# Performance work log

Hardware: AMD Instinct MI355X
Metric: run time of the kernel (lower is better)

Reference implementation:

```python
import jax, jax.numpy as jnp
import numpy as np

INPUT_DIM = 1024
OUTPUT_DIM = 1024
DEGREE = 8


def pentanacci_basis(x, degree):
    # x: [B, I] (already sigmoided). Returns [B, I, degree+1].
    # P0 = 0, P1 = 1, P2 = x, P3 = x, P4 = x^2,
    # Pn = x*P(n-1) + P(n-2) + P(n-3) + P(n-4) + P(n-5) for n >= 5
    zeros = jnp.zeros_like(x)
    ones = jnp.ones_like(x)
    seeds = [zeros, ones, x, x, x * x]
    basis = seeds[: degree + 1]
    for n in range(5, degree + 1):
        basis.append(x * basis[n - 1] + basis[n - 2] + basis[n - 3]
                     + basis[n - 4] + basis[n - 5])
    return jnp.stack(basis, axis=-1)


def setup_inputs() -> dict:
    key = jax.random.key(0)
    kx, kw = jax.random.split(key)
    x = jax.random.normal(kx, (4096, INPUT_DIM), dtype=jnp.float32)
    std = 1.0 / (INPUT_DIM * (DEGREE + 1))
    coeffs = std * jax.random.normal(kw, (INPUT_DIM, OUTPUT_DIM, DEGREE + 1),
                                     dtype=jnp.float32)
    return {"x": x, "coeffs": coeffs}


def reference(x, coeffs):
    degree = coeffs.shape[-1] - 1
    xs = jax.nn.sigmoid(x)                      # [B, I]
    basis = pentanacci_basis(xs, degree)        # [B, I, D+1]
    y = jnp.einsum('bid,iod->bo', basis, coeffs)  # [B, O]
    return y
```

## Files before the change

### kernel.cpp

```cpp
#include <hip/hip_runtime.h>
#include <stdint.h>

#define M_DIM 4096
#define I_DIM 1024
#define O_DIM 1024
#define KB 6
#define K_DIM (I_DIM * KB)
#define SPLITS 4

typedef __attribute__((ext_vector_type(8))) short short8;
typedef __attribute__((ext_vector_type(4))) float f32x4;
typedef __attribute__((ext_vector_type(4))) unsigned int u32x4;
typedef __attribute__((ext_vector_type(4))) float hfloat4;

__device__ __forceinline__ unsigned short f2bf(float f) {
  union { float f; unsigned int u; } v; v.f = f;
  unsigned int u = v.u;
  unsigned int r = (u + 0x7FFFu + ((u >> 16) & 1u)) >> 16;
  return (unsigned short)r;
}

__global__ __launch_bounds__(256) void k_basis(const float* __restrict__ x,
                                               unsigned short* __restrict__ A) {
  int t = blockIdx.x * 256 + threadIdx.x;
  long e0 = (long)t * 8;
  const hfloat4* xp = (const hfloat4*)(x + e0);
  hfloat4 v0 = xp[0], v1 = xp[1];
  float xv[8];
  xv[0]=v0[0]; xv[1]=v0[1]; xv[2]=v0[2]; xv[3]=v0[3];
  xv[4]=v1[0]; xv[5]=v1[1]; xv[6]=v1[2]; xv[7]=v1[3];
  unsigned short outv[48];
#pragma unroll
  for (int e = 0; e < 8; ++e) {
    float s  = 1.0f / (1.0f + __expf(-xv[e]));
    float b2 = s, b3 = s, b4 = s * s;
    float b5 = fmaf(s, b4, b3 + b2 + 1.0f);
    float b6 = fmaf(s, b5, b4 + b3 + b2 + 1.0f);
    float b7 = fmaf(s, b6, b5 + b4 + b3 + b2);
    float b8 = fmaf(s, b7, b6 + b5 + b4 + b3);
    outv[e*6+0] = f2bf(s);
    outv[e*6+1] = f2bf(b4);
    outv[e*6+2] = f2bf(b5);
    outv[e*6+3] = f2bf(b6);
    outv[e*6+4] = f2bf(b7);
    outv[e*6+5] = f2bf(b8);
  }
  u32x4* dst = (u32x4*)(A + e0 * KB);
  const u32x4* srcv = (const u32x4*)outv;
#pragma unroll
  for (int q = 0; q < 6; ++q) dst[q] = srcv[q];
}

__global__ __launch_bounds__(256) void k_coef(const float* __restrict__ C,
                                              unsigned short* __restrict__ Bt,
                                              float* __restrict__ partB) {
  __shared__ unsigned short tile[32 * 192];
  __shared__ float bred[256];
  int i0 = blockIdx.x * 32, o0 = blockIdx.y * 32;
  int t = threadIdx.x;
  int ol = t & 31, ig = t >> 5;
  float bsum = 0.f;
#pragma unroll
  for (int r = 0; r < 4; ++r) {
    int il = ig + r * 8;
    const float* p = C + (size_t)(i0 + il) * (O_DIM * 9) + (size_t)(o0 + ol) * 9;
    float c1 = p[1];
    float c2 = p[2], c3 = p[3], c4 = p[4], c5 = p[5], c6 = p[6], c7 = p[7], c8 = p[8];
    bsum += c1;
    unsigned short* q = &tile[ol * 192 + il * 6];
    q[0] = f2bf(c2 + c3);
    q[1] = f2bf(c4);
    q[2] = f2bf(c5);
    q[3] = f2bf(c6);
    q[4] = f2bf(c7);
    q[5] = f2bf(c8);
  }
  bred[t] = bsum;
  __syncthreads();
  if (t < 32) {
    float s = 0.f;
#pragma unroll
    for (int g = 0; g < 8; ++g) s += bred[g * 32 + t];
    partB[(size_t)blockIdx.x * O_DIM + o0 + t] = s;
  }
  const u32x4* lsrc = (const u32x4*)tile;
#pragma unroll
  for (int r = 0; r < 3; ++r) {
    int c = t + r * 256;
    int row = c / 24, off = c % 24;
    u32x4* gdst = (u32x4*)(Bt + (size_t)(o0 + row) * K_DIM + (size_t)i0 * 6 + off * 8);
    *gdst = lsrc[c];
  }
}

__global__ __launch_bounds__(256) void k_bias2(const float* __restrict__ partB,
                                               float* __restrict__ bias) {
  int o = blockIdx.x * 256 + threadIdx.x;
  float s = 0.f;
#pragma unroll
  for (int ib = 0; ib < 32; ++ib) s += partB[(size_t)ib * O_DIM + o];
  bias[o] = s;
}

#define SBAR __builtin_amdgcn_sched_barrier(0)

template<bool SPLIT>
__global__ __launch_bounds__(512, 2) void k_gemm8(const unsigned short* __restrict__ A,
                                                  const unsigned short* __restrict__ B,
                                                  const float* __restrict__ bias,
                                                  float* __restrict__ dst) {
  constexpr int CK = SPLIT ? (K_DIM / SPLITS) : K_DIM;
  constexpr int NT = CK / 64;
  constexpr int PPX = SPLIT ? 8 : 2;
  __shared__ char lds[131072];
  const int tid = threadIdx.x;
  const int lane = tid & 63, wid = tid >> 6;
  const int wm = wid >> 2, wn = wid & 3;
  const int l15 = lane & 15, lk = lane >> 4, l7 = lane & 7;
  const int flat = blockIdx.x + (blockIdx.y << 2) + (blockIdx.z << 6);
  const int xcd = flat & 7, slot = flat >> 3;
  const int panel = xcd * PPX + (slot >> 2);
  const int xn = slot & 3;
  const int ym = panel & 15, zk = panel >> 4;
  const int m0 = ym * 256, n0 = xn * 256;
  const size_t kb = (size_t)zk * CK;
  const int srow = tid >> 3;
  const int cg8 = (((tid & 7) ^ ((tid >> 3) & 7)) * 8);
  const int cx0 = (lk ^ l7) * 16;
  const int cx1 = ((4 + lk) ^ l7) * 16;
  const int arow = wm * 128 + l15;
  const int brow = wn * 64 + l15;

  auto gload = [&](const unsigned short* s, int ldsoff) {
    __builtin_amdgcn_global_load_lds((const __attribute__((address_space(1))) void*)s,
        (__attribute__((address_space(3))) void*)(lds + ldsoff), 16, 0, 0);
  };
  auto stageA = [&](int buf, int h, int kt2) {
    const unsigned short* s = A + (size_t)(m0 + h * 128 + srow) * K_DIM + kb + (size_t)kt2 * 64 + cg8;
    int d = buf * 65536 + h * 16384 + tid * 16;
    gload(s, d);
    gload(s + (size_t)64 * K_DIM, d + 8192);
  };
  auto stageB = [&](int buf, int h, int kt2) {
    const unsigned short* s = B + (size_t)(n0 + h * 128 + srow) * K_DIM + kb + (size_t)kt2 * 64 + cg8;
    int d = buf * 65536 + 32768 + h * 16384 + tid * 16;
    gload(s, d);
    gload(s + (size_t)64 * K_DIM, d + 8192);
  };

  short8 af[4][2], bf0[2][2], bf1[2][2];
  f32x4 acc[8][4];
#pragma unroll
  for (int i = 0; i < 8; ++i)
#pragma unroll
    for (int n = 0; n < 4; ++n)
#pragma unroll
      for (int j = 0; j < 4; ++j) acc[i][n][j] = 0.f;

  auto loadA = [&](int buf, int h) {
#pragma unroll
    for (int mm = 0; mm < 4; ++mm) {
      int rb = buf * 65536 + (arow + h * 64 + mm * 16) * 128;
      af[mm][0] = *(const short8*)(lds + rb + cx0);
      af[mm][1] = *(const short8*)(lds + rb + cx1);
    }
  };
  auto loadB = [&](int buf, int g, short8 (&bfx)[2][2]) {
#pragma unroll
    for (int nn = 0; nn < 2; ++nn) {
      int rb = buf * 65536 + 32768 + (brow + g * 32 + nn * 16) * 128;
      bfx[nn][0] = *(const short8*)(lds + rb + cx0);
      bfx[nn][1] = *(const short8*)(lds + rb + cx1);
    }
  };
  auto quad = [&](int h, int g, short8 (&bfx)[2][2]) {
#pragma unroll
    for (int mm = 0; mm < 4; ++mm)
#pragma unroll
      for (int nn = 0; nn < 2; ++nn)
#pragma unroll
        for (int kc = 0; kc < 2; ++kc)
          acc[h * 4 + mm][g * 2 + nn] =
              __builtin_amdgcn_mfma_f32_16x16x32_bf16(af[mm][kc], bfx[nn][kc],
                                                      acc[h * 4 + mm][g * 2 + nn], 0, 0, 0);
  };
  auto sync1 = [&]() {
    SBAR; __builtin_amdgcn_s_barrier();
    asm volatile("s_waitcnt lgkmcnt(0)" ::: "memory"); SBAR;
    __builtin_amdgcn_s_setprio(1);
  };
  auto endp = [&]() {
    __builtin_amdgcn_s_setprio(0); SBAR;
  };

  stageA(0, 0, 0); stageA(0, 1, 0); stageB(0, 0, 0); stageB(0, 1, 0);
  stageB(1, 0, 1); stageB(1, 1, 1);
  asm volatile("s_waitcnt vmcnt(4)" ::: "memory"); SBAR;
  __builtin_amdgcn_s_barrier(); SBAR;

#pragma unroll 1
  for (int kt = 0; kt < NT; ++kt) {
    const int buf = kt & 1, nb = buf ^ 1;
    loadA(buf, 0); loadB(buf, 0, bf0);
    if (kt + 1 < NT) stageA(nb, 1, kt + 1);
    sync1(); quad(0, 0, bf0); endp();
    loadB(buf, 1, bf1);
    if (kt + 1 < NT) stageA(nb, 0, kt + 1);
    sync1(); quad(0, 1, bf1); endp();
    loadA(buf, 1);
    if (kt + 2 < NT) stageB(buf, 0, kt + 2);
    sync1(); quad(1, 1, bf1); endp();
    if (kt + 2 < NT) stageB(buf, 1, kt + 2);
    sync1(); quad(1, 0, bf0); endp();
    if (kt + 1 < NT) {
      if (kt + 2 < NT) asm volatile("s_waitcnt vmcnt(4)" ::: "memory");
      else             asm volatile("s_waitcnt vmcnt(0)" ::: "memory");
      SBAR;
      __builtin_amdgcn_s_barrier(); SBAR;
    }
  }

  float* base = SPLIT ? (dst + (size_t)zk * ((size_t)M_DIM * O_DIM)) : dst;
#pragma unroll
  for (int mi = 0; mi < 8; ++mi) {
    int r0 = m0 + wm * 128 + mi * 16 + (lk << 2);
#pragma unroll
    for (int ni = 0; ni < 4; ++ni) {
      int col = n0 + wn * 64 + ni * 16 + l15;
      float bv = SPLIT ? 0.f : bias[col];
#pragma unroll
      for (int j = 0; j < 4; ++j)
        base[(size_t)(r0 + j) * O_DIM + col] = acc[mi][ni][j] + bv;
    }
  }
}

__global__ __launch_bounds__(256) void k_reduce(const float* __restrict__ part,
                                                const float* __restrict__ bias,
                                                float* __restrict__ out) {
  size_t t = (size_t)blockIdx.x * 256 + threadIdx.x;
  size_t idx = t * 4;
  const size_t P = (size_t)M_DIM * O_DIM;
  f32x4 s0 = *(const f32x4*)(part + idx);
  f32x4 s1 = *(const f32x4*)(part + P + idx);
  f32x4 s2 = *(const f32x4*)(part + 2 * P + idx);
  f32x4 s3 = *(const f32x4*)(part + 3 * P + idx);
  f32x4 bv = *(const f32x4*)(bias + (idx & (O_DIM - 1)));
  f32x4 r;
#pragma unroll
  for (int j = 0; j < 4; ++j) r[j] = ((s0[j] + s1[j]) + (s2[j] + s3[j])) + bv[j];
  *(f32x4*)(out + idx) = r;
}

extern "C" void kernel_launch(void* const* d_in, const int* in_sizes, int n_in,
                              void* d_out, int out_size, void* d_ws, size_t ws_size,
                              hipStream_t stream) {
  const float* x      = (const float*)d_in[0];
  const float* coeffs = (const float*)d_in[1];
  float* out = (float*)d_out;
  char* ws = (char*)d_ws;
  const size_t offA     = 0;
  const size_t offB     = 50331648;
  const size_t offBias  = offB + 12582912;
  const size_t offPartB = offBias + 4096;
  const size_t offPart  = offPartB + 131072;
  const size_t needSplit = offPart + (size_t)SPLITS * M_DIM * O_DIM * 4;

  unsigned short* A  = (unsigned short*)(ws + offA);
  unsigned short* Bt = (unsigned short*)(ws + offB);
  float* bias        = (float*)(ws + offBias);
  float* partB       = (float*)(ws + offPartB);
  float* part        = (float*)(ws + offPart);

  k_basis<<<2048, 256, 0, stream>>>(x, A);
  k_coef<<<dim3(32, 32), 256, 0, stream>>>(coeffs, Bt, partB);
  k_bias2<<<4, 256, 0, stream>>>(partB, bias);

  if (ws_size >= needSplit) {
    k_gemm8<true><<<dim3(O_DIM / 256, M_DIM / 256, SPLITS), 512, 0, stream>>>(A, Bt, bias, part);
    k_reduce<<<(M_DIM * O_DIM) / (256 * 4), 256, 0, stream>>>(part, bias, out);
  } else {
    k_gemm8<false><<<dim3(O_DIM / 256, M_DIM / 256, 1), 512, 0, stream>>>(A, Bt, bias, out);
  }
}
```

Baseline: 95.61 us.

## Store split-K partials in fp16 and merge basis/coef prep kernels

The split-K GEMM partial sums are now written as fp16 instead of fp32, halving the partial-buffer write and reduce-read traffic. The reduce kernel now handles 8 elements per thread with fp16 loads. Separately, the basis and coefficient preparation kernels are merged into one launch that branches on block index, removing a launch gap. Storing partials in fp16 loses precision and range in the intermediate sums.

```diff
diff --git a/kernel.cpp b/kernel.cpp
--- a/kernel.cpp
+++ b/kernel.cpp
@@ -12,6 +12,7 @@
 typedef __attribute__((ext_vector_type(4))) float f32x4;
 typedef __attribute__((ext_vector_type(4))) unsigned int u32x4;
 typedef __attribute__((ext_vector_type(4))) float hfloat4;
+typedef __attribute__((ext_vector_type(8))) _Float16 h16x8;
 
 __device__ __forceinline__ unsigned short f2bf(float f) {
   union { float f; unsigned int u; } v; v.f = f;
@@ -20,76 +21,79 @@
   return (unsigned short)r;
 }
 
-__global__ __launch_bounds__(256) void k_basis(const float* __restrict__ x,
-                                               unsigned short* __restrict__ A) {
-  int t = blockIdx.x * 256 + threadIdx.x;
-  long e0 = (long)t * 8;
-  const hfloat4* xp = (const hfloat4*)(x + e0);
-  hfloat4 v0 = xp[0], v1 = xp[1];
-  float xv[8];
-  xv[0]=v0[0]; xv[1]=v0[1]; xv[2]=v0[2]; xv[3]=v0[3];
-  xv[4]=v1[0]; xv[5]=v1[1]; xv[6]=v1[2]; xv[7]=v1[3];
-  unsigned short outv[48];
-#pragma unroll
-  for (int e = 0; e < 8; ++e) {
-    float s  = 1.0f / (1.0f + __expf(-xv[e]));
-    float b2 = s, b3 = s, b4 = s * s;
-    float b5 = fmaf(s, b4, b3 + b2 + 1.0f);
-    float b6 = fmaf(s, b5, b4 + b3 + b2 + 1.0f);
-    float b7 = fmaf(s, b6, b5 + b4 + b3 + b2);
-    float b8 = fmaf(s, b7, b6 + b5 + b4 + b3);
-    outv[e*6+0] = f2bf(s);
-    outv[e*6+1] = f2bf(b4);
-    outv[e*6+2] = f2bf(b5);
-    outv[e*6+3] = f2bf(b6);
-    outv[e*6+4] = f2bf(b7);
-    outv[e*6+5] = f2bf(b8);
-  }
-  u32x4* dst = (u32x4*)(A + e0 * KB);
-  const u32x4* srcv = (const u32x4*)outv;
-#pragma unroll
-  for (int q = 0; q < 6; ++q) dst[q] = srcv[q];
-}
-
-__global__ __launch_bounds__(256) void k_coef(const float* __restrict__ C,
+__global__ __launch_bounds__(256) void k_prep(const float* __restrict__ x,
+                                              const float* __restrict__ C,
+                                              unsigned short* __restrict__ A,
                                               unsigned short* __restrict__ Bt,
                                               float* __restrict__ partB) {
-  __shared__ unsigned short tile[32 * 192];
-  __shared__ float bred[256];
-  int i0 = blockIdx.x * 32, o0 = blockIdx.y * 32;
-  int t = threadIdx.x;
-  int ol = t & 31, ig = t >> 5;
-  float bsum = 0.f;
-#pragma unroll
-  for (int r = 0; r < 4; ++r) {
-    int il = ig + r * 8;
-    const float* p = C + (size_t)(i0 + il) * (O_DIM * 9) + (size_t)(o0 + ol) * 9;
-    float c1 = p[1];
-    float c2 = p[2], c3 = p[3], c4 = p[4], c5 = p[5], c6 = p[6], c7 = p[7], c8 = p[8];
-    bsum += c1;
-    unsigned short* q = &tile[ol * 192 + il * 6];
-    q[0] = f2bf(c2 + c3);
-    q[1] = f2bf(c4);
-    q[2] = f2bf(c5);
-    q[3] = f2bf(c6);
-    q[4] = f2bf(c7);
-    q[5] = f2bf(c8);
-  }
-  bred[t] = bsum;
-  __syncthreads();
-  if (t < 32) {
-    float s = 0.f;
-#pragma unroll
-    for (int g = 0; g < 8; ++g) s += bred[g * 32 + t];
-    partB[(size_t)blockIdx.x * O_DIM + o0 + t] = s;
-  }
-  const u32x4* lsrc = (const u32x4*)tile;
-#pragma unroll
-  for (int r = 0; r < 3; ++r) {
-    int c = t + r * 256;
-    int row = c / 24, off = c % 24;
-    u32x4* gdst = (u32x4*)(Bt + (size_t)(o0 + row) * K_DIM + (size_t)i0 * 6 + off * 8);
-    *gdst = lsrc[c];
+  const int bid = blockIdx.x;
+  if (bid < 2048) {
+    int t = bid * 256 + threadIdx.x;
+    long e0 = (long)t * 8;
+    const hfloat4* xp = (const hfloat4*)(x + e0);
+    hfloat4 v0 = xp[0], v1 = xp[1];
+    float xv[8];
+    xv[0]=v0[0]; xv[1]=v0[1]; xv[2]=v0[2]; xv[3]=v0[3];
+    xv[4]=v1[0]; xv[5]=v1[1]; xv[6]=v1[2]; xv[7]=v1[3];
+    unsigned short outv[48];
+#pragma unroll
+    for (int e = 0; e < 8; ++e) {
+      float s  = 1.0f / (1.0f + __expf(-xv[e]));
+      float b2 = s, b3 = s, b4 = s * s;
+      float b5 = fmaf(s, b4, b3 + b2 + 1.0f);
+      float b6 = fmaf(s, b5, b4 + b3 + b2 + 1.0f);
+      float b7 = fmaf(s, b6, b5 + b4 + b3 + b2);
+      float b8 = fmaf(s, b7, b6 + b5 + b4 + b3);
+      outv[e*6+0] = f2bf(s);
+      outv[e*6+1] = f2bf(b4);
+      outv[e*6+2] = f2bf(b5);
+      outv[e*6+3] = f2bf(b6);
+      outv[e*6+4] = f2bf(b7);
+      outv[e*6+5] = f2bf(b8);
+    }
+    u32x4* dst = (u32x4*)(A + e0 * KB);
+    const u32x4* srcv = (const u32x4*)outv;
+#pragma unroll
+    for (int q = 0; q < 6; ++q) dst[q] = srcv[q];
+  } else {
+    __shared__ unsigned short tile[32 * 192];
+    __shared__ float bred[256];
+    int b = bid - 2048;
+    int i0 = (b & 31) * 32, o0 = (b >> 5) * 32;
+    int t = threadIdx.x;
+    int ol = t & 31, ig = t >> 5;
+    float bsum = 0.f;
+#pragma unroll
+    for (int r = 0; r < 4; ++r) {
+      int il = ig + r * 8;
+      const float* p = C + (size_t)(i0 + il) * (O_DIM * 9) + (size_t)(o0 + ol) * 9;
+      float c1 = p[1];
+      float c2 = p[2], c3 = p[3], c4 = p[4], c5 = p[5], c6 = p[6], c7 = p[7], c8 = p[8];
+      bsum += c1;
+      unsigned short* q = &tile[ol * 192 + il * 6];
+      q[0] = f2bf(c2 + c3);
+      q[1] = f2bf(c4);
+      q[2] = f2bf(c5);
+      q[3] = f2bf(c6);
+      q[4] = f2bf(c7);
+      q[5] = f2bf(c8);
+    }
+    bred[t] = bsum;
+    __syncthreads();
+    if (t < 32) {
+      float s = 0.f;
+#pragma unroll
+      for (int g = 0; g < 8; ++g) s += bred[g * 32 + t];
+      partB[(size_t)(b & 31) * O_DIM + o0 + t] = s;
+    }
+    const u32x4* lsrc = (const u32x4*)tile;
+#pragma unroll
+    for (int r = 0; r < 3; ++r) {
+      int c = t + r * 256;
+      int row = c / 24, off = c % 24;
+      u32x4* gdst = (u32x4*)(Bt + (size_t)(o0 + row) * K_DIM + (size_t)i0 * 6 + off * 8);
+      *gdst = lsrc[c];
+    }
   }
 }
 
@@ -108,7 +112,7 @@
 __global__ __launch_bounds__(512, 2) void k_gemm8(const unsigned short* __restrict__ A,
                                                   const unsigned short* __restrict__ B,
                                                   const float* __restrict__ bias,
-                                                  float* __restrict__ dst) {
+                                                  void* __restrict__ dst) {
   constexpr int CK = SPLIT ? (K_DIM / SPLITS) : K_DIM;
   constexpr int NT = CK / 64;
   constexpr int PPX = SPLIT ? 8 : 2;
@@ -220,36 +224,57 @@
     }
   }
 
-  float* base = SPLIT ? (dst + (size_t)zk * ((size_t)M_DIM * O_DIM)) : dst;
-#pragma unroll
-  for (int mi = 0; mi < 8; ++mi) {
-    int r0 = m0 + wm * 128 + mi * 16 + (lk << 2);
-#pragma unroll
-    for (int ni = 0; ni < 4; ++ni) {
-      int col = n0 + wn * 64 + ni * 16 + l15;
-      float bv = SPLIT ? 0.f : bias[col];
-#pragma unroll
-      for (int j = 0; j < 4; ++j)
-        base[(size_t)(r0 + j) * O_DIM + col] = acc[mi][ni][j] + bv;
-    }
-  }
-}
-
-__global__ __launch_bounds__(256) void k_reduce(const float* __restrict__ part,
+  if (SPLIT) {
+    _Float16* base = (_Float16*)dst + (size_t)zk * ((size_t)M_DIM * O_DIM);
+#pragma unroll
+    for (int mi = 0; mi < 8; ++mi) {
+      int r0 = m0 + wm * 128 + mi * 16 + (lk << 2);
+#pragma unroll
+      for (int ni = 0; ni < 4; ++ni) {
+        int col = n0 + wn * 64 + ni * 16 + l15;
+#pragma unroll
+        for (int j = 0; j < 4; ++j)
+          base[(size_t)(r0 + j) * O_DIM + col] = (_Float16)acc[mi][ni][j];
+      }
+    }
+  } else {
+    float* base = (float*)dst;
+#pragma unroll
+    for (int mi = 0; mi < 8; ++mi) {
+      int r0 = m0 + wm * 128 + mi * 16 + (lk << 2);
+#pragma unroll
+      for (int ni = 0; ni < 4; ++ni) {
+        int col = n0 + wn * 64 + ni * 16 + l15;
+        float bv = bias[col];
+#pragma unroll
+        for (int j = 0; j < 4; ++j)
+          base[(size_t)(r0 + j) * O_DIM + col] = acc[mi][ni][j] + bv;
+      }
+    }
+  }
+}
+
+__global__ __launch_bounds__(256) void k_reduce(const _Float16* __restrict__ part,
                                                 const float* __restrict__ bias,
                                                 float* __restrict__ out) {
   size_t t = (size_t)blockIdx.x * 256 + threadIdx.x;
-  size_t idx = t * 4;
+  size_t idx = t * 8;
   const size_t P = (size_t)M_DIM * O_DIM;
-  f32x4 s0 = *(const f32x4*)(part + idx);
-  f32x4 s1 = *(const f32x4*)(part + P + idx);
-  f32x4 s2 = *(const f32x4*)(part + 2 * P + idx);
-  f32x4 s3 = *(const f32x4*)(part + 3 * P + idx);
-  f32x4 bv = *(const f32x4*)(bias + (idx & (O_DIM - 1)));
-  f32x4 r;
-#pragma unroll
-  for (int j = 0; j < 4; ++j) r[j] = ((s0[j] + s1[j]) + (s2[j] + s3[j])) + bv[j];
-  *(f32x4*)(out + idx) = r;
+  h16x8 s0 = *(const h16x8*)(part + idx);
+  h16x8 s1 = *(const h16x8*)(part + P + idx);
+  h16x8 s2 = *(const h16x8*)(part + 2 * P + idx);
+  h16x8 s3 = *(const h16x8*)(part + 3 * P + idx);
+  size_t bo = idx & (O_DIM - 1);
+  f32x4 b0 = *(const f32x4*)(bias + bo);
+  f32x4 b1 = *(const f32x4*)(bias + bo + 4);
+  f32x4 r0, r1;
+#pragma unroll
+  for (int j = 0; j < 4; ++j) {
+    r0[j] = (((float)s0[j] + (float)s1[j]) + ((float)s2[j] + (float)s3[j])) + b0[j];
+    r1[j] = (((float)s0[j+4] + (float)s1[j+4]) + ((float)s2[j+4] + (float)s3[j+4])) + b1[j];
+  }
+  *(f32x4*)(out + idx) = r0;
+  *(f32x4*)(out + idx + 4) = r1;
 }
 
 extern "C" void kernel_launch(void* const* d_in, const int* in_sizes, int n_in,
@@ -264,22 +289,21 @@
   const size_t offBias  = offB + 12582912;
   const size_t offPartB = offBias + 4096;
   const size_t offPart  = offPartB + 131072;
-  const size_t needSplit = offPart + (size_t)SPLITS * M_DIM * O_DIM * 4;
+  const size_t needSplit = offPart + (size_t)SPLITS * M_DIM * O_DIM * 2;
 
   unsigned short* A  = (unsigned short*)(ws + offA);
   unsigned short* Bt = (unsigned short*)(ws + offB);
   float* bias        = (float*)(ws + offBias);
   float* partB       = (float*)(ws + offPartB);
-  float* part        = (float*)(ws + offPart);
-
-  k_basis<<<2048, 256, 0, stream>>>(x, A);
-  k_coef<<<dim3(32, 32), 256, 0, stream>>>(coeffs, Bt, partB);
+  _Float16* part     = (_Float16*)(ws + offPart);
+
+  k_prep<<<3072, 256, 0, stream>>>(x, coeffs, A, Bt, partB);
   k_bias2<<<4, 256, 0, stream>>>(partB, bias);
 
   if (ws_size >= needSplit) {
-    k_gemm8<true><<<dim3(O_DIM / 256, M_DIM / 256, SPLITS), 512, 0, stream>>>(A, Bt, bias, part);
-    k_reduce<<<(M_DIM * O_DIM) / (256 * 4), 256, 0, stream>>>(part, bias, out);
+    k_gemm8<true><<<dim3(O_DIM / 256, M_DIM / 256, SPLITS), 512, 0, stream>>>(A, Bt, bias, (void*)part);
+    k_reduce<<<(M_DIM * O_DIM) / (256 * 8), 256, 0, stream>>>(part, bias, out);
   } else {
-    k_gemm8<false><<<dim3(O_DIM / 256, M_DIM / 256, 1), 512, 0, stream>>>(A, Bt, bias, out);
-  }
-}
+    k_gemm8<false><<<dim3(O_DIM / 256, M_DIM / 256, 1), 512, 0, stream>>>(A, Bt, bias, (void*)out);
+  }
+}
```

Result: faster. 88.77 us (-7.2%).
